# Performance work log

Hardware: AMD Instinct MI355X
Metric: run time of the kernel (lower is better)

## Reference

```python
import jax, jax.numpy as jnp
import numpy as np

K = 76          # model dim = 6 + 30 + 30 + 10 (concat of modality embeddings)
H = 8           # heads; per-head dim == K (wide attention variant)
D = 6           # depth
T = 1024        # seq_length (frames)
B = 8           # batch
C = 2           # num_classes
EPS = 1e-5


def setup_inputs() -> dict:
    key = jax.random.key(0)
    ks = jax.random.split(key, 24)
    rn = lambda k, shape, s=0.02: (jax.random.normal(k, shape, jnp.float32) * s)
    return {
        # forward inputs (per-frame multimodal features)
        "v": jax.random.normal(ks[0], (B, T, 6), jnp.float32),
        "x": jax.random.normal(ks[1], (B, T, 137), jnp.float32),
        "y": jax.random.normal(ks[2], (B, T, 113), jnp.float32),
        "z": jax.random.normal(ks[3], (B, T, 35), jnp.float32),
        # modality embed linears (stored (in, out); torch does x @ W.T)
        "W_hp": rn(ks[4], (6, 6)),     "b_hp": jnp.zeros((6,), jnp.float32),
        "W_lm": rn(ks[5], (137, 30)),  "b_lm": jnp.zeros((30,), jnp.float32),
        "W_el": rn(ks[6], (113, 30)),  "b_el": jnp.zeros((30,), jnp.float32),
        "W_au": rn(ks[7], (35, 10)),   "b_au": jnp.zeros((10,), jnp.float32),
        "pos_emb": rn(ks[8], (T, K)),
        # per-block params stacked over depth for lax.scan
        "Wq": rn(ks[9], (D, K, H * K)),
        "Wk": rn(ks[10], (D, K, H * K)),
        "Wv": rn(ks[11], (D, K, H * K)),
        "Wu": rn(ks[12], (D, H * K, K)), "bu": jnp.zeros((D, K), jnp.float32),
        "ln1_s": jnp.ones((D, K), jnp.float32), "ln1_b": jnp.zeros((D, K), jnp.float32),
        "W1": rn(ks[13], (D, K, 4 * K)), "b1": jnp.zeros((D, 4 * K), jnp.float32),
        "W2": rn(ks[14], (D, 4 * K, K)), "b2": jnp.zeros((D, K), jnp.float32),
        "ln2_s": jnp.ones((D, K), jnp.float32), "ln2_b": jnp.zeros((D, K), jnp.float32),
        "W_out": rn(ks[15], (K, C)), "b_out": jnp.zeros((C,), jnp.float32),
    }


def _layernorm(h, s, b):
    mu = jnp.mean(h, axis=-1, keepdims=True)
    var = jnp.mean(jnp.square(h - mu), axis=-1, keepdims=True)
    return (h - mu) * jax.lax.rsqrt(var + EPS) * s + b


def reference(v, x, y, z,
              W_hp, b_hp, W_lm, b_lm, W_el, b_el, W_au, b_au,
              pos_emb, Wq, Wk, Wv, Wu, bu, ln1_s, ln1_b,
              W1, b1, W2, b2, ln2_s, ln2_b, W_out, b_out):
    b, t = v.shape[0], v.shape[1]
    tokens = jnp.concatenate([
        v @ W_hp + b_hp,
        x @ W_lm + b_lm,
        y @ W_el + b_el,
        z @ W_au + b_au,
    ], axis=2)                                   # (b, t, K)
    h = tokens + pos_emb[None, :, :]
    scale = 1.0 / np.sqrt(K)                     # dot / sqrt(e), e == k

    def block(hh, p):
        wq, wk, wv, wu, bu_, l1s, l1b, w1, b1_, w2, b2_, l2s, l2b = p
        # (b, t, H*K) -> (b, H, t, K); per-head dim is full K here
        q = (hh @ wq).reshape(b, t, H, K).transpose(0, 2, 1, 3)
        k_ = (hh @ wk).reshape(b, t, H, K).transpose(0, 2, 1, 3)
        vv = (hh @ wv).reshape(b, t, H, K).transpose(0, 2, 1, 3)
        dot = jax.nn.softmax(jnp.einsum('bhte,bhse->bhts', q, k_) * scale, axis=-1)
        att = jnp.einsum('bhts,bhse->bhte', dot, vv)        # (b, H, t, K)
        att = att.transpose(0, 2, 1, 3).reshape(b, t, H * K)
        att = att @ wu + bu_                                # unify heads -> (b, t, K)
        h1 = _layernorm(att + hh, l1s, l1b)
        ff = jax.nn.relu(h1 @ w1 + b1_) @ w2 + b2_
        return _layernorm(ff + h1, l2s, l2b), None

    h, _ = jax.lax.scan(
        block, h,
        (Wq, Wk, Wv, Wu, bu, ln1_s, ln1_b, W1, b1, W2, b2, ln2_s, ln2_b))
    return h @ W_out + b_out                     # (b, t, num_classes)
```

## Files before the change

kernel.cpp:

```cpp
#include <hip/hip_runtime.h>
#include <hip/hip_bf16.h>
#include <math.h>

#define B_   8
#define T_   1024
#define K_   76
#define KP_  96
#define H_   8
#define D_   6
#define C_   2
#define HK_  608
#define QKLD_ 640
#define FF_  304
#define FFP_ 320
#define EK_  320
#define BT_  8192
#define EPS_ 1e-5f
#define SCL2_ (0.11470786693528088f * 1.4426950408889634f)

typedef unsigned short u16;
typedef unsigned int u32;
typedef short bf16x8 __attribute__((ext_vector_type(8)));
typedef float f32x4 __attribute__((ext_vector_type(4)));

__device__ __forceinline__ u16 f2b(float f) {
  __hip_bfloat16 h = __float2bfloat16(f);
  return *reinterpret_cast<u16*>(&h);
}
__device__ __forceinline__ float b2f(u16 u) {
  __hip_bfloat16 h = *reinterpret_cast<__hip_bfloat16*>(&u);
  return __bfloat162float(h);
}
__device__ __forceinline__ u32 pack2(float a, float b) {
  __hip_bfloat162 t = __float22bfloat162_rn(make_float2(a, b));
  return *reinterpret_cast<u32*>(&t);
}

#define PER_L_ 304128ULL
__global__ __launch_bounds__(256) void wconv_kernel(
    const float* __restrict__ Wq, const float* __restrict__ Wk, const float* __restrict__ Wv,
    const float* __restrict__ Wu, const float* __restrict__ W1, const float* __restrict__ W2,
    u16* __restrict__ WT) {
  __shared__ float Ls[32][65];
  int zz = blockIdx.y;
  int d = zz / 6, wt = zz % 6;
  const float* in; int Kd, Nsrc, Nalloc, Kp; u16* out;
  size_t lb = (size_t)d * PER_L_;
  switch (wt) {
    case 0: in = Wq + (size_t)d*K_*HK_; Kd=K_;  Nsrc=HK_; Nalloc=640; Kp=KP_;  out = WT + lb;          break;
    case 1: in = Wk + (size_t)d*K_*HK_; Kd=K_;  Nsrc=HK_; Nalloc=640; Kp=KP_;  out = WT + lb + 61440;  break;
    case 2: in = Wv + (size_t)d*K_*HK_; Kd=K_;  Nsrc=HK_; Nalloc=640; Kp=KP_;  out = WT + lb + 122880; break;
    case 3: in = Wu + (size_t)d*HK_*K_; Kd=HK_; Nsrc=K_;  Nalloc=96;  Kp=HK_;  out = WT + lb + 184320; break;
    case 4: in = W1 + (size_t)d*K_*FF_; Kd=K_;  Nsrc=FF_; Nalloc=320; Kp=KP_;  out = WT + lb + 242688; break;
    default:in = W2 + (size_t)d*FF_*K_; Kd=FF_; Nsrc=K_;  Nalloc=96;  Kp=FFP_; out = WT + lb + 273408; break;
  }
  int tiles_k = Kp / 32;
  int tiles_n = (Nalloc + 63) / 64;
  int tile = blockIdx.x;
  if (tile >= tiles_k * tiles_n) return;
  int tn = tile / tiles_k, tk = tile % tiles_k;
  int n0 = tn * 64, k0 = tk * 32;
  for (int i = threadIdx.x; i < 2048; i += 256) {
    int kk = i >> 6, nn = i & 63;
    int gk = k0 + kk, gn = n0 + nn;
    int srccol = gn;
    if (wt < 3) {
      int hh8 = gn / 80, ft = gn - hh8 * 80;
      srccol = (ft < 76) ? (hh8 * 76 + ft) : -1;
    }
    Ls[kk][nn] = (gk < Kd && srccol >= 0 && srccol < Nsrc) ? in[(size_t)gk * Nsrc + srccol] : 0.f;
  }
  __syncthreads();
  for (int i = threadIdx.x; i < 2048; i += 256) {
    int nn = i >> 5, kk = i & 31;
    int gn = n0 + nn;
    if (gn < Nalloc) out[(size_t)gn * Kp + k0 + kk] = f2b(Ls[kk][nn]);
  }
}

__global__ void wembed_kernel(const float* __restrict__ W_hp, const float* __restrict__ b_hp,
                              const float* __restrict__ W_lm, const float* __restrict__ b_lm,
                              const float* __restrict__ W_el, const float* __restrict__ b_el,
                              const float* __restrict__ W_au, const float* __restrict__ b_au,
                              u16* __restrict__ WE) {
  int idx = blockIdx.x * 256 + threadIdx.x;
  if (idx >= 96 * EK_) return;
  int n = idx / EK_, kk = idx % EK_;
  float val = 0.f;
  if (n < 76) {
    if (kk < 6) { if (n < 6) val = W_hp[kk * 6 + n]; }
    else if (kk < 143) { int i = kk - 6; if (n >= 6 && n < 36) val = W_lm[i * 30 + (n - 6)]; }
    else if (kk < 256) { int i = kk - 143; if (n >= 36 && n < 66) val = W_el[i * 30 + (n - 36)]; }
    else if (kk < 291) { int i = kk - 256; if (n >= 66) val = W_au[i * 10 + (n - 66)]; }
    else if (kk == 291) {
      val = (n < 6) ? b_hp[n] : (n < 36) ? b_lm[n - 6] : (n < 66) ? b_el[n - 36] : b_au[n - 66];
    }
  }
  WE[idx] = f2b(val);
}

__global__ void pack_kernel(const float* __restrict__ v, const float* __restrict__ x,
                            const float* __restrict__ y, const float* __restrict__ z,
                            u16* __restrict__ xin) {
  int idx = blockIdx.x * 256 + threadIdx.x;
  if (idx >= BT_ * (EK_ / 2)) return;
  int bt = idx / (EK_ / 2), dc = idx % (EK_ / 2);
  int c0 = dc * 2;
  auto fetch = [&](int c) -> float {
    if (c < 6) return v[bt * 6 + c];
    if (c < 143) return x[bt * 137 + c - 6];
    if (c < 256) return y[bt * 113 + c - 143];
    if (c < 291) return z[bt * 35 + c - 256];
    if (c == 291) return 1.0f;
    return 0.f;
  };
  ((u32*)xin)[idx] = pack2(fetch(c0), fetch(c0 + 1));
}

template<int RT, int CT, int KSTEPS, int RELU, int TPB>
__global__ __launch_bounds__(TPB) void gemm_kernel(
    const u16* __restrict__ A, int lda,
    const u16* __restrict__ Wt, int ldw, unsigned long long wstride,
    const float* __restrict__ bias,
    u16* __restrict__ Cc, int ldc, int N,
    int ksplit, int klen, unsigned long long osplit,
    float cs,
    u16* __restrict__ vbt,
    const float* __restrict__ pos) {
  __shared__ u16 Bs[CT * 16 * 56];
  const int tid = threadIdx.x;
  const int w = tid >> 6, lane = tid & 63;
  const int r = lane & 15, g = lane >> 4;
  const int n0 = blockIdx.x * CT * 16;
  const int m0 = blockIdx.y * (TPB / 64) * 16 * RT;
  const int z = blockIdx.z;
  const int k0 = z * ksplit;
  const int kend = k0 + klen;
  const u16* Wz = Wt + (size_t)z * wstride;
  const float* bias_eff = (z == 0) ? bias : nullptr;
  const float csz = (z == 0) ? cs : 1.f;
  u16* Cz = Cc + (size_t)z * osplit;
  constexpr int NB = (CT * 64 + TPB - 1) / TPB;

  const f32x4 fz = {0.f, 0.f, 0.f, 0.f};
  f32x4 acc[RT][CT];
  #pragma unroll
  for (int rt = 0; rt < RT; rt++)
    #pragma unroll
    for (int ct = 0; ct < CT; ct++) acc[rt][ct] = fz;

  bf16x8 a_all[RT][KSTEPS];
  #pragma unroll
  for (int rt = 0; rt < RT; rt++) {
    const u16* arow = A + (size_t)(m0 + (w * RT + rt) * 16 + r) * lda;
    #pragma unroll
    for (int ks = 0; ks < KSTEPS; ks++) {
      int kA = k0 + ks * 32 + g * 8;
      if (kA < kend) a_all[rt][ks] = *(const bf16x8*)(arow + kA);
      else a_all[rt][ks] = bf16x8{0, 0, 0, 0, 0, 0, 0, 0};
    }
  }

  uint4 bpre[NB];
  auto loadB = [&](int ks) {
    int kk = k0 + ks * 32;
    #pragma unroll
    for (int i0 = 0; i0 < NB; i0++) {
      int idx = tid + i0 * TPB;
      bpre[i0] = make_uint4(0, 0, 0, 0);
      if (idx < CT * 64) {
        int nn = idx >> 2, kc = idx & 3;
        if (kk + kc * 8 < kend)
          bpre[i0] = *(const uint4*)(Wz + (size_t)(n0 + nn) * ldw + kk + kc * 8);
      }
    }
  };
  loadB(0);

  for (int ks = 0; ks < KSTEPS; ks++) {
    __syncthreads();
    #pragma unroll
    for (int i0 = 0; i0 < NB; i0++) {
      int idx = tid + i0 * TPB;
      if (idx < CT * 64) {
        int nn = idx >> 2, kc = idx & 3;
        *(uint4*)&Bs[nn * 56 + (((kc ^ (nn & 3)) << 3))] = bpre[i0];
      }
    }
    __syncthreads();
    if (ks + 1 < KSTEPS) loadB(ks + 1);
    #pragma unroll
    for (int ct = 0; ct < CT; ct++) {
      bf16x8 bb = *(const bf16x8*)&Bs[(ct * 16 + r) * 56 + (((g ^ (r & 3)) << 3))];
      #pragma unroll
      for (int rt = 0; rt < RT; rt++)
        acc[rt][ct] = __builtin_amdgcn_mfma_f32_16x16x32_bf16(a_all[rt][ks], bb, acc[rt][ct], 0, 0, 0);
    }
  }

  if (vbt && z == 2) {
    #pragma unroll
    for (int rt = 0; rt < RT; rt++) {
      #pragma unroll
      for (int ct = 0; ct < CT; ct++) {
        int feat = ct * 16 + r;
        int token = m0 + (w * RT + rt) * 16 + g * 4;
        int bb_ = token >> 10, tt = token & 1023;
        ushort4 pk;
        if (feat < 76) {
          pk.x = f2b(acc[rt][ct][0]); pk.y = f2b(acc[rt][ct][1]);
          pk.z = f2b(acc[rt][ct][2]); pk.w = f2b(acc[rt][ct][3]);
        } else {
          pk = make_ushort4(0, 0, 0, 0);
        }
        *(ushort4*)(vbt + (((size_t)(bb_ * 8 + blockIdx.x) * 80 + feat) << 10) + tt) = pk;
      }
    }
  } else {
    #pragma unroll
    for (int rt = 0; rt < RT; rt++) {
      #pragma unroll
      for (int ct = 0; ct < CT; ct++) {
        int col = n0 + ct * 16 + r;
        if (col < ldc) {
          #pragma unroll
          for (int reg = 0; reg < 4; reg++) {
            int row = m0 + (w * RT + rt) * 16 + g * 4 + reg;
            float val = acc[rt][ct][reg] * csz;
            if (bias_eff && col < N) val += bias_eff[col];
            if (pos && col < N) val += pos[(row & (T_ - 1)) * K_ + col];
            if (RELU) val = fmaxf(val, 0.f);
            Cz[(size_t)row * ldc + col] = f2b(val);
          }
        }
      }
    }
  }
}

__global__ __launch_bounds__(64) void ffn_kernel(
    const u16* __restrict__ att, const u16* __restrict__ WuT, const float* __restrict__ bu,
    const u16* __restrict__ hres, const float* __restrict__ l1s, const float* __restrict__ l1b,
    const u16* __restrict__ W1T, const float* __restrict__ b1,
    const u16* __restrict__ W2T, const float* __restrict__ b2,
    const float* __restrict__ l2s, const float* __restrict__ l2b,
    u16* __restrict__ hout) {
  __shared__ u16 Bs[6 * 16 * 56];
  __shared__ u16 h1s[16 * 104];
  __shared__ u16 ffs[16 * 328];
  const int lane = threadIdx.x & 63;
  const int r = lane & 15, g = lane >> 4;
  const int m0 = blockIdx.x * 16;
  const f32x4 fz = {0.f, 0.f, 0.f, 0.f};

  u16 resv[4][6];
  #pragma unroll
  for (int reg = 0; reg < 4; reg++)
    #pragma unroll
    for (int ct = 0; ct < 6; ct++)
      resv[reg][ct] = hres[(size_t)(m0 + g * 4 + reg) * KP_ + ct * 16 + r];

  bf16x8 a1[19];
  {
    const u16* arow = att + (size_t)(m0 + r) * HK_;
    #pragma unroll
    for (int ks = 0; ks < 19; ks++) a1[ks] = *(const bf16x8*)(arow + ks * 32 + g * 8);
  }
  f32x4 acc1[6];
  #pragma unroll
  for (int ct = 0; ct < 6; ct++) acc1[ct] = fz;
  {
    uint4 bpre[6];
    auto loadB1 = [&](int ks) {
      #pragma unroll
      for (int i0 = 0; i0 < 6; i0++) {
        int idx = lane + i0 * 64;
        int nn = idx >> 2, kc = idx & 3;
        bpre[i0] = *(const uint4*)(WuT + (size_t)nn * HK_ + ks * 32 + kc * 8);
      }
    };
    loadB1(0);
    for (int ks = 0; ks < 19; ks++) {
      #pragma unroll
      for (int i0 = 0; i0 < 6; i0++) {
        int idx = lane + i0 * 64;
        int nn = idx >> 2, kc = idx & 3;
        *(uint4*)&Bs[nn * 56 + ((kc ^ (nn & 3)) << 3)] = bpre[i0];
      }
      if (ks + 1 < 19) loadB1(ks + 1);
      #pragma unroll
      for (int ct = 0; ct < 6; ct++) {
        bf16x8 bb = *(const bf16x8*)&Bs[(ct * 16 + r) * 56 + ((g ^ (r & 3)) << 3)];
        acc1[ct] = __builtin_amdgcn_mfma_f32_16x16x32_bf16(a1[ks], bb, acc1[ct], 0, 0, 0);
      }
    }
  }
  #pragma unroll
  for (int reg = 0; reg < 4; reg++) {
    float vals[6];
    float s = 0.f, s2 = 0.f;
    #pragma unroll
    for (int ct = 0; ct < 6; ct++) {
      int col = ct * 16 + r;
      float val = 0.f;
      if (col < K_) {
        val = acc1[ct][reg] + bu[col] + b2f(resv[reg][ct]);
        s += val; s2 += val * val;
      }
      vals[ct] = val;
    }
    #pragma unroll
    for (int m = 1; m < 16; m <<= 1) { s += __shfl_xor(s, m); s2 += __shfl_xor(s2, m); }
    float mu = s * (1.f / 76.f);
    float rstd = rsqrtf(s2 * (1.f / 76.f) - mu * mu + EPS_);
    #pragma unroll
    for (int ct = 0; ct < 6; ct++) {
      int col = ct * 16 + r;
      u16 ov = 0;
      if (col < K_) ov = f2b((vals[ct] - mu) * rstd * l1s[col] + l1b[col]);
      h1s[(g * 4 + reg) * 104 + col] = ov;
    }
  }

  bf16x8 a2[3];
  #pragma unroll
  for (int ks = 0; ks < 3; ks++)
    a2[ks] = *(const bf16x8*)&h1s[r * 104 + ks * 32 + g * 8];
  f32x4 acc2[20];
  #pragma unroll
  for (int ct = 0; ct < 20; ct++) acc2[ct] = fz;
  #pragma unroll
  for (int ks = 0; ks < 3; ks++) {
    bf16x8 bb[20];
    #pragma unroll
    for (int ct = 0; ct < 20; ct++)
      bb[ct] = *(const bf16x8*)(W1T + (size_t)(ct * 16 + r) * KP_ + ks * 32 + g * 8);
    #pragma unroll
    for (int ct = 0; ct < 20; ct++)
      acc2[ct] = __builtin_amdgcn_mfma_f32_16x16x32_bf16(a2[ks], bb[ct], acc2[ct], 0, 0, 0);
  }
  #pragma unroll
  for (int reg = 0; reg < 4; reg++)
    #pragma unroll
    for (int ct = 0; ct < 20; ct++) {
      int col = ct * 16 + r;
      float val = acc2[ct][reg] + ((col < FF_) ? b1[col] : 0.f);
      ffs[(g * 4 + reg) * 328 + col] = f2b(fmaxf(val, 0.f));
    }

  bf16x8 a3[10];
  #pragma unroll
  for (int ks = 0; ks < 10; ks++)
    a3[ks] = *(const bf16x8*)&ffs[r * 328 + ks * 32 + g * 8];
  f32x4 acc3[6];
  #pragma unroll
  for (int ct = 0; ct < 6; ct++) acc3[ct] = fz;
  {
    uint4 bpre[6];
    auto loadB3 = [&](int ks) {
      #pragma unroll
      for (int i0 = 0; i0 < 6; i0++) {
        int idx = lane + i0 * 64;
        int nn = idx >> 2, kc = idx & 3;
        bpre[i0] = *(const uint4*)(W2T + (size_t)nn * FFP_ + ks * 32 + kc * 8);
      }
    };
    loadB3(0);
    for (int ks = 0; ks < 10; ks++) {
      #pragma unroll
      for (int i0 = 0; i0 < 6; i0++) {
        int idx = lane + i0 * 64;
        int nn = idx >> 2, kc = idx & 3;
        *(uint4*)&Bs[nn * 56 + ((kc ^ (nn & 3)) << 3)] = bpre[i0];
      }
      if (ks + 1 < 10) loadB3(ks + 1);
      #pragma unroll
      for (int ct = 0; ct < 6; ct++) {
        bf16x8 bb = *(const bf16x8*)&Bs[(ct * 16 + r) * 56 + ((g ^ (r & 3)) << 3)];
        acc3[ct] = __builtin_amdgcn_mfma_f32_16x16x32_bf16(a3[ks], bb, acc3[ct], 0, 0, 0);
      }
    }
  }
  #pragma unroll
  for (int reg = 0; reg < 4; reg++) {
    float vals[6];
    float s = 0.f, s2 = 0.f;
    #pragma unroll
    for (int ct = 0; ct < 6; ct++) {
      int col = ct * 16 + r;
      float val = 0.f;
      if (col < K_) {
        val = acc3[ct][reg] + b2[col] + b2f(h1s[(g * 4 + reg) * 104 + col]);
        s += val; s2 += val * val;
      }
      vals[ct] = val;
    }
    #pragma unroll
    for (int m = 1; m < 16; m <<= 1) { s += __shfl_xor(s, m); s2 += __shfl_xor(s2, m); }
    float mu = s * (1.f / 76.f);
    float rstd = rsqrtf(s2 * (1.f / 76.f) - mu * mu + EPS_);
    u16* outr = hout + (size_t)(m0 + g * 4 + reg) * KP_;
    #pragma unroll
    for (int ct = 0; ct < 6; ct++) {
      int col = ct * 16 + r;
      u16 ov = 0;
      if (col < K_) ov = f2b((vals[ct] - mu) * rstd * l2s[col] + l2b[col]);
      outr[col] = ov;
    }
  }
}

__global__ __launch_bounds__(256, 3) void attn_kernel(const u16* __restrict__ q,
                                                      const u16* __restrict__ k,
                                                      const u16* __restrict__ vbt,
                                                      u16* __restrict__ att) {
  __shared__ u16 Ks[64 * 104];
  __shared__ u16 Vs[80 * 72];
  __shared__ u32 Psw[128 * 36];
  const int bid = blockIdx.x;
  const int hh = bid & 7, b = (bid >> 3) & 7, qt = bid >> 6;
  const int tid = threadIdx.x;
  const int w = tid >> 6, lane = tid & 63;
  const int r = lane & 15, g = lane >> 4;
  const int qbase = b * T_ + qt * 128;

  bf16x8 aq[2][3];
  #pragma unroll
  for (int rt = 0; rt < 2; rt++) {
    const u16* qsrc = q + (size_t)(qbase + w * 32 + rt * 16 + r) * QKLD_ + hh * 80;
    #pragma unroll
    for (int ks = 0; ks < 3; ks++) {
      int e0 = ks * 32 + g * 8;
      aq[rt][ks] = (e0 < 80) ? *(const bf16x8*)(qsrc + e0) : bf16x8{0, 0, 0, 0, 0, 0, 0, 0};
    }
  }

  const int krow = tid >> 2, kq4 = tid & 3;
  uint4 kpre[3], vpre[3];
  auto stage_load = [&](int kt) {
    const int kb = b * T_ + kt * 64;
    const u16* ksrc = k + (size_t)(kb + krow) * QKLD_ + hh * 80;
    #pragma unroll
    for (int i = 0; i < 3; i++) {
      int c = kq4 + 4 * i;
      kpre[i] = (c < 10) ? *(const uint4*)(ksrc + c * 8) : make_uint4(0, 0, 0, 0);
    }
    const u16* vsrc = vbt + (((size_t)(b * 8 + hh) * 80) << 10) + kt * 64;
    #pragma unroll
    for (int p = 0; p < 3; p++) {
      int idx = tid + p * 256;
      vpre[p] = (idx < 640) ? *(const uint4*)(vsrc + ((size_t)(idx >> 3) << 10) + (idx & 7) * 8)
                            : make_uint4(0, 0, 0, 0);
    }
  };
  auto stage_write = [&]() {
    #pragma unroll
    for (int i = 0; i < 3; i++) {
      int c = kq4 + 4 * i;
      *(uint4*)&Ks[krow * 104 + c * 8] = kpre[i];
    }
    #pragma unroll
    for (int p = 0; p < 3; p++) {
      int idx = tid + p * 256;
      if (idx < 640)
        *(uint4*)&Vs[(idx >> 3) * 72 + (idx & 7) * 8] = vpre[p];
    }
  };

  u32* Pw = Psw + w * 32 * 36;

  const f32x4 fz = {0.f, 0.f, 0.f, 0.f};
  f32x4 o[2][5];
  float ls[2] = {0.f, 0.f};
  #pragma unroll
  for (int rt = 0; rt < 2; rt++)
    #pragma unroll
    for (int i = 0; i < 5; i++) o[rt][i] = fz;

  stage_load(0);

  for (int kt = 0; kt < 16; kt++) {
    __syncthreads();
    stage_write();
    __syncthreads();
    if (kt < 15) stage_load(kt + 1);

    f32x4 st[2][4];
    #pragma unroll
    for (int ct = 0; ct < 4; ct++) { st[0][ct] = fz; st[1][ct] = fz; }
    __builtin_amdgcn_s_setprio(1);
    #pragma unroll
    for (int ct = 0; ct < 4; ct++) {
      #pragma unroll
      for (int ks = 0; ks < 3; ks++) {
        bf16x8 ak = *(const bf16x8*)&Ks[(ct * 16 + r) * 104 + ks * 32 + g * 8];
        st[0][ct] = __builtin_amdgcn_mfma_f32_16x16x32_bf16(ak, aq[0][ks], st[0][ct], 0, 0, 0);
        st[1][ct] = __builtin_amdgcn_mfma_f32_16x16x32_bf16(ak, aq[1][ks], st[1][ct], 0, 0, 0);
      }
    }
    __builtin_amdgcn_s_setprio(0);

    #pragma unroll
    for (int rt = 0; rt < 2; rt++) {
      float rs = 0.f;
      u32 pk[8];
      #pragma unroll
      for (int ct = 0; ct < 4; ct++) {
        float p0 = exp2f(st[rt][ct][0]), p1 = exp2f(st[rt][ct][1]);
        float p2 = exp2f(st[rt][ct][2]), p3 = exp2f(st[rt][ct][3]);
        rs += (p0 + p1) + (p2 + p3);
        pk[ct * 2] = pack2(p0, p1);
        pk[ct * 2 + 1] = pack2(p2, p3);
      }
      ls[rt] += rs;
      u32* pw = Pw + (rt * 16 + r) * 36;
      #pragma unroll
      for (int ct = 0; ct < 4; ct++)
        *(uint2*)(pw + ct * 8 + g * 2) = make_uint2(pk[ct * 2], pk[ct * 2 + 1]);
    }

    bf16x8 pa[2][2];
    #pragma unroll
    for (int rt = 0; rt < 2; rt++) {
      const u32* pr = Pw + (rt * 16 + r) * 36;
      #pragma unroll
      for (int ks = 0; ks < 2; ks++) {
        uint4 t = *(const uint4*)(pr + ks * 16 + g * 4);
        pa[rt][ks] = *reinterpret_cast<bf16x8*>(&t);
      }
    }
    __builtin_amdgcn_s_setprio(1);
    #pragma unroll
    for (int ks = 0; ks < 2; ks++) {
      #pragma unroll
      for (int c5 = 0; c5 < 5; c5++) {
        bf16x8 av = *(const bf16x8*)&Vs[(c5 * 16 + r) * 72 + ks * 32 + g * 8];
        #pragma unroll
        for (int rt = 0; rt < 2; rt++)
          o[rt][c5] = __builtin_amdgcn_mfma_f32_16x16x32_bf16(av, pa[rt][ks], o[rt][c5], 0, 0, 0);
      }
    }
    __builtin_amdgcn_s_setprio(0);
  }

  #pragma unroll
  for (int rt = 0; rt < 2; rt++) {
    ls[rt] += __shfl_xor(ls[rt], 16);
    ls[rt] += __shfl_xor(ls[rt], 32);
    float inv = 1.f / ls[rt];
    int token = qbase + w * 32 + rt * 16 + r;
    #pragma unroll
    for (int c5 = 0; c5 < 5; c5++) {
      if (c5 == 4 && g == 3) continue;
      ushort4 pk4;
      pk4.x = f2b(o[rt][c5][0] * inv);
      pk4.y = f2b(o[rt][c5][1] * inv);
      pk4.z = f2b(o[rt][c5][2] * inv);
      pk4.w = f2b(o[rt][c5][3] * inv);
      *(ushort4*)&att[(size_t)token * HK_ + hh * 76 + c5 * 16 + g * 4] = pk4;
    }
  }
}

__global__ void out_kernel(const u16* __restrict__ h, const float* __restrict__ W,
                           const float* __restrict__ bias, float* __restrict__ out) {
  int bt = blockIdx.x * 256 + threadIdx.x;
  if (bt >= BT_) return;
  const u32* hr = (const u32*)(h + (size_t)bt * KP_);
  float acc0 = bias[0], acc1 = bias[1];
  #pragma unroll 4
  for (int d = 0; d < 38; d++) {
    u32 h2 = hr[d];
    float f0 = b2f((u16)(h2 & 0xffff)), f1 = b2f((u16)(h2 >> 16));
    acc0 += f0 * W[(2 * d) * 2] + f1 * W[(2 * d + 1) * 2];
    acc1 += f0 * W[(2 * d) * 2 + 1] + f1 * W[(2 * d + 1) * 2 + 1];
  }
  out[bt * 2] = acc0;
  out[bt * 2 + 1] = acc1;
}

extern "C" void kernel_launch(void* const* d_in, const int* in_sizes, int n_in,
                              void* d_out, int out_size, void* d_ws, size_t ws_size,
                              hipStream_t stream) {
  const float* v    = (const float*)d_in[0];
  const float* x    = (const float*)d_in[1];
  const float* y    = (const float*)d_in[2];
  const float* z    = (const float*)d_in[3];
  const float* W_hp = (const float*)d_in[4];
  const float* b_hp = (const float*)d_in[5];
  const float* W_lm = (const float*)d_in[6];
  const float* b_lm = (const float*)d_in[7];
  const float* W_el = (const float*)d_in[8];
  const float* b_el = (const float*)d_in[9];
  const float* W_au = (const float*)d_in[10];
  const float* b_au = (const float*)d_in[11];
  const float* pos  = (const float*)d_in[12];
  const float* Wq   = (const float*)d_in[13];
  const float* Wk   = (const float*)d_in[14];
  const float* Wv   = (const float*)d_in[15];
  const float* Wu   = (const float*)d_in[16];
  const float* bu   = (const float*)d_in[17];
  const float* ln1s = (const float*)d_in[18];
  const float* ln1b = (const float*)d_in[19];
  const float* W1   = (const float*)d_in[20];
  const float* b1   = (const float*)d_in[21];
  const float* W2   = (const float*)d_in[22];
  const float* b2   = (const float*)d_in[23];
  const float* ln2s = (const float*)d_in[24];
  const float* ln2b = (const float*)d_in[25];
  const float* Wout = (const float*)d_in[26];
  const float* bout = (const float*)d_in[27];

  u16* ws  = (u16*)d_ws;
  u16* WT  = ws;
  u16* WE  = WT + 1824768;
  u16* h   = WE + 30720;
  u16* xin = h + 786432;
  u16* qb  = xin + 2621440;
  u16* kb  = qb + 5242880;
  u16* vbt = kb + 5242880;
  u16* att = vbt + 5242880;
  u16* h1  = att + 4980736;

  wconv_kernel<<<dim3(38, 36), 256, 0, stream>>>(Wq, Wk, Wv, Wu, W1, W2, WT);
  wembed_kernel<<<(96 * EK_ + 255) / 256, 256, 0, stream>>>(
      W_hp, b_hp, W_lm, b_lm, W_el, b_el, W_au, b_au, WE);
  pack_kernel<<<(BT_ * (EK_ / 2) + 255) / 256, 256, 0, stream>>>(v, x, y, z, xin);
  gemm_kernel<1, 6, 10, 0, 128><<<dim3(1, 256, 1), 128, 0, stream>>>(
      xin, EK_, WE, EK_, 0ULL, nullptr, h, KP_, K_, 0, EK_, 0ULL,
      1.f, nullptr, pos);

  for (int d = 0; d < D_; d++) {
    u16* WTd = WT + (size_t)d * PER_L_;
    const float* bu_d = bu + (size_t)d * K_;
    const float* l1s  = ln1s + (size_t)d * K_;
    const float* l1b  = ln1b + (size_t)d * K_;
    const float* b1_d = b1 + (size_t)d * FF_;
    const float* b2_d = b2 + (size_t)d * K_;
    const float* l2s  = ln2s + (size_t)d * K_;
    const float* l2b  = ln2b + (size_t)d * K_;

    gemm_kernel<2, 5, 3, 0, 256><<<dim3(8, 64, 3), 256, 0, stream>>>(
        h, KP_, WTd, KP_, 61440ULL, nullptr, qb, QKLD_, QKLD_, 0, KP_, 5242880ULL,
        SCL2_, vbt, nullptr);
    attn_kernel<<<dim3(512), 256, 0, stream>>>(qb, kb, vbt, att);
    ffn_kernel<<<dim3(512), 64, 0, stream>>>(
        att, WTd + 184320, bu_d, h, l1s, l1b,
        WTd + 242688, b1_d, WTd + 273408, b2_d, l2s, l2b, h);
  }

  out_kernel<<<(BT_ + 255) / 256, 256, 0, stream>>>(h, Wout, bout, (float*)d_out);
}
```

Before: 571.3 us.

## Split attention KV range across two wave groups and merge partials in LDS

Attention blocks now use 512 threads: two groups of four waves each process half of the key/value sequence for the same 128 queries. Partial outputs and row sums are combined through shared memory before normalisation and write-out. This aims to halve the serial KV loop per block and raise the number of waves in flight, at the cost of more LDS per block, an extra merge step and launch bounds that allow only one block per CU.

```diff
diff --git a/kernel.cpp b/kernel.cpp
--- a/kernel.cpp
+++ b/kernel.cpp
@@ -410,24 +410,26 @@
   }
 }
 
-__global__ __launch_bounds__(256, 3) void attn_kernel(const u16* __restrict__ q,
+__global__ __launch_bounds__(512, 1) void attn_kernel(const u16* __restrict__ q,
                                                       const u16* __restrict__ k,
                                                       const u16* __restrict__ vbt,
                                                       u16* __restrict__ att) {
-  __shared__ u16 Ks[64 * 104];
-  __shared__ u16 Vs[80 * 72];
-  __shared__ u32 Psw[128 * 36];
+  __shared__ u16 KV[2][12416];
+  __shared__ u32 Psw[9216];
   const int bid = blockIdx.x;
   const int hh = bid & 7, b = (bid >> 3) & 7, qt = bid >> 6;
   const int tid = threadIdx.x;
   const int w = tid >> 6, lane = tid & 63;
   const int r = lane & 15, g = lane >> 4;
+  const int kvh = w >> 2, wq = w & 3;
   const int qbase = b * T_ + qt * 128;
+  u16* Ks = KV[kvh];
+  u16* Vs = KV[kvh] + 6656;
 
   bf16x8 aq[2][3];
   #pragma unroll
   for (int rt = 0; rt < 2; rt++) {
-    const u16* qsrc = q + (size_t)(qbase + w * 32 + rt * 16 + r) * QKLD_ + hh * 80;
+    const u16* qsrc = q + (size_t)(qbase + wq * 32 + rt * 16 + r) * QKLD_ + hh * 80;
     #pragma unroll
     for (int ks = 0; ks < 3; ks++) {
       int e0 = ks * 32 + g * 8;
@@ -435,20 +437,21 @@
     }
   }
 
-  const int krow = tid >> 2, kq4 = tid & 3;
+  const int th = tid & 255;
+  const int krow = th >> 2, kq4 = th & 3;
   uint4 kpre[3], vpre[3];
   auto stage_load = [&](int kt) {
-    const int kb = b * T_ + kt * 64;
+    const int kb = b * T_ + kvh * 512 + kt * 64;
     const u16* ksrc = k + (size_t)(kb + krow) * QKLD_ + hh * 80;
     #pragma unroll
     for (int i = 0; i < 3; i++) {
       int c = kq4 + 4 * i;
       kpre[i] = (c < 10) ? *(const uint4*)(ksrc + c * 8) : make_uint4(0, 0, 0, 0);
     }
-    const u16* vsrc = vbt + (((size_t)(b * 8 + hh) * 80) << 10) + kt * 64;
+    const u16* vsrc = vbt + (((size_t)(b * 8 + hh) * 80) << 10) + kvh * 512 + kt * 64;
     #pragma unroll
     for (int p = 0; p < 3; p++) {
-      int idx = tid + p * 256;
+      int idx = th + p * 256;
       vpre[p] = (idx < 640) ? *(const uint4*)(vsrc + ((size_t)(idx >> 3) << 10) + (idx & 7) * 8)
                             : make_uint4(0, 0, 0, 0);
     }
@@ -461,7 +464,7 @@
     }
     #pragma unroll
     for (int p = 0; p < 3; p++) {
-      int idx = tid + p * 256;
+      int idx = th + p * 256;
       if (idx < 640)
         *(uint4*)&Vs[(idx >> 3) * 72 + (idx & 7) * 8] = vpre[p];
     }
@@ -479,11 +482,11 @@
 
   stage_load(0);
 
-  for (int kt = 0; kt < 16; kt++) {
+  for (int kt = 0; kt < 8; kt++) {
     __syncthreads();
     stage_write();
     __syncthreads();
-    if (kt < 15) stage_load(kt + 1);
+    if (kt < 7) stage_load(kt + 1);
 
     f32x4 st[2][4];
     #pragma unroll
@@ -547,17 +550,38 @@
   for (int rt = 0; rt < 2; rt++) {
     ls[rt] += __shfl_xor(ls[rt], 16);
     ls[rt] += __shfl_xor(ls[rt], 32);
-    float inv = 1.f / ls[rt];
-    int token = qbase + w * 32 + rt * 16 + r;
-    #pragma unroll
-    for (int c5 = 0; c5 < 5; c5++) {
-      if (c5 == 4 && g == 3) continue;
-      ushort4 pk4;
-      pk4.x = f2b(o[rt][c5][0] * inv);
-      pk4.y = f2b(o[rt][c5][1] * inv);
-      pk4.z = f2b(o[rt][c5][2] * inv);
-      pk4.w = f2b(o[rt][c5][3] * inv);
-      *(ushort4*)&att[(size_t)token * HK_ + hh * 76 + c5 * 16 + g * 4] = pk4;
+  }
+
+  __syncthreads();
+  float* cb = (float*)KV;
+  if (kvh == 1) {
+    float* slot = cb + (size_t)(wq * 64 + lane) * 44;
+    #pragma unroll
+    for (int rt = 0; rt < 2; rt++)
+      #pragma unroll
+      for (int c5 = 0; c5 < 5; c5++)
+        *(f32x4*)(slot + (rt * 5 + c5) * 4) = o[rt][c5];
+    slot[40] = ls[0];
+    slot[41] = ls[1];
+  }
+  __syncthreads();
+  if (kvh == 0) {
+    const float* slot = cb + (size_t)(wq * 64 + lane) * 44;
+    #pragma unroll
+    for (int rt = 0; rt < 2; rt++) {
+      float inv = 1.f / (ls[rt] + slot[40 + rt]);
+      int token = qbase + wq * 32 + rt * 16 + r;
+      #pragma unroll
+      for (int c5 = 0; c5 < 5; c5++) {
+        if (c5 == 4 && g == 3) continue;
+        f32x4 ot = o[rt][c5] + *(const f32x4*)(slot + (rt * 5 + c5) * 4);
+        ushort4 pk4;
+        pk4.x = f2b(ot[0] * inv);
+        pk4.y = f2b(ot[1] * inv);
+        pk4.z = f2b(ot[2] * inv);
+        pk4.w = f2b(ot[3] * inv);
+        *(ushort4*)&att[(size_t)token * HK_ + hh * 76 + c5 * 16 + g * 4] = pk4;
+      }
     }
   }
 }
@@ -620,7 +644,6 @@
   u16* kb  = qb + 5242880;
   u16* vbt = kb + 5242880;
   u16* att = vbt + 5242880;
-  u16* h1  = att + 4980736;
 
   wconv_kernel<<<dim3(38, 36), 256, 0, stream>>>(Wq, Wk, Wv, Wu, W1, W2, WT);
   wembed_kernel<<<(96 * EK_ + 255) / 256, 256, 0, stream>>>(
@@ -643,7 +666,7 @@
     gemm_kernel<2, 5, 3, 0, 256><<<dim3(8, 64, 3), 256, 0, stream>>>(
         h, KP_, WTd, KP_, 61440ULL, nullptr, qb, QKLD_, QKLD_, 0, KP_, 5242880ULL,
         SCL2_, vbt, nullptr);
-    attn_kernel<<<dim3(512), 256, 0, stream>>>(qb, kb, vbt, att);
+    attn_kernel<<<dim3(512), 512, 0, stream>>>(qb, kb, vbt, att);
     ffn_kernel<<<dim3(512), 64, 0, stream>>>(
         att, WTd + 184320, bu_d, h, l1s, l1b,
         WTd + 242688, b1_d, WTd + 273408, b2_d, l2s, l2b, h);
```

Result: slower. 609.6 us (+6.7%).
